# Performance work log

Measured on AMD Instinct MI355X. Metric: run time of the kernel, lower is better.

The kernel has to match this reference:

```python
import jax, jax.numpy as jnp
import numpy as np

B, U, N0, N1, E, H = 8, 8192, 64, 64, 128, 8
S = N0 * N1


def setup_inputs() -> dict:
    key = jax.random.key(0)
    ks = jax.random.split(key, 9)
    # regular grid over [-1, 1]^2 (meshgrid, 'ij' indexing)
    c0 = jnp.linspace(-1.0, 1.0, N0)
    c1 = jnp.linspace(-1.0, 1.0, N1)
    g0, g1 = jnp.meshgrid(c0, c1, indexing='ij')
    xc_on_grid = jnp.broadcast_to(jnp.stack([g0, g1], -1), (B, N0, N1, 2))
    xc_off_grid = jax.random.uniform(ks[0], (B, U, 2), minval=-1.0, maxval=1.0)
    zc_off_grid = jax.random.normal(ks[1], (B, U, E))
    zc_on_grid = jax.random.normal(ks[2], (B, N0, N1, E))
    latents = jax.random.normal(ks[3], (N0, N1, E))
    fake_embedding = jax.random.normal(ks[4], (E,))
    sc = 1.0 / np.sqrt(E).astype(np.float32)
    Wq = jax.random.normal(ks[5], (E, E)) * sc
    Wk = jax.random.normal(ks[6], (E, E)) * sc
    Wv = jax.random.normal(ks[7], (E, E)) * sc
    Wo = jax.random.normal(ks[8], (E, E)) * sc
    return dict(xc_off_grid=xc_off_grid, xc_on_grid=xc_on_grid,
                zc_off_grid=zc_off_grid, zc_on_grid=zc_on_grid,
                latents=latents, fake_embedding=fake_embedding,
                Wq=Wq, Wk=Wk, Wv=Wv, Wo=Wo, used_modality=0)


def _nearest_idx(x, x_grid):
    # nearest cell on a regular grid, flattened row-major (k=1 of nearest_gridded_neighbours)
    n0, n1 = x_grid.shape[1], x_grid.shape[2]
    c0 = x_grid[:, :, 0, 0]   # [B, n0]
    c1 = x_grid[:, 0, :, 1]   # [B, n1]
    sp0 = (c0[:, 1] - c0[:, 0])[:, None]
    sp1 = (c1[:, 1] - c1[:, 0])[:, None]
    i0 = jnp.clip(jnp.round((x[..., 0] - c0[:, :1]) / sp0), 0, n0 - 1)
    i1 = jnp.clip(jnp.round((x[..., 1] - c1[:, :1]) / sp1), 0, n1 - 1)
    return (i0 * n1 + i1).astype(jnp.int32)


def _cumcount(nearest):
    # duplicate-count within each grid cell via linear-recurrence associative scan
    # (same math as the torch complex-log scan: x_t = a_t*x_{t-1} + b_t, a=b=same-flag)
    sort_idx = jnp.argsort(nearest, axis=1, stable=True)
    ns = jnp.take_along_axis(nearest, sort_idx, axis=1)
    same = (ns == jnp.roll(ns, 1, axis=1)).astype(jnp.float32)
    same = same.at[:, 0].set(0.0)

    def combine(c1, c2):
        a1, b1 = c1
        a2, b2 = c2
        return a1 * a2, a2 * b1 + b2

    _, cc = jax.lax.associative_scan(combine, (same, same), axis=1)
    unsort = jnp.argsort(sort_idx, axis=1, stable=True)
    return jnp.take_along_axis(jnp.round(cc), unsort, axis=1).astype(jnp.int32)


def _mhca(q, kv, mask, Wq, Wk, Wv, Wo):
    # q: [N,1,E], kv: [N,P,E], mask: [N,1,P] (True = attend)
    N, P, Ed = kv.shape
    dh = Ed // H
    qh = (q @ Wq).reshape(N, 1, H, dh).transpose(0, 2, 1, 3)
    kh = (kv @ Wk).reshape(N, P, H, dh).transpose(0, 2, 1, 3)
    vh = (kv @ Wv).reshape(N, P, H, dh).transpose(0, 2, 1, 3)
    scores = jnp.einsum('nhqd,nhkd->nhqk', qh, kh) / jnp.sqrt(jnp.asarray(dh, qh.dtype))
    scores = jnp.where(mask[:, None, :, :], scores, -jnp.inf)
    attn = jax.nn.softmax(scores, axis=-1)
    out = jnp.einsum('nhqk,nhkd->nhqd', attn, vh)
    return out.transpose(0, 2, 1, 3).reshape(N, 1, Ed) @ Wo


def reference(xc_off_grid, xc_on_grid, zc_off_grid, zc_on_grid, latents,
              fake_embedding, Wq, Wk, Wv, Wo, used_modality):
    # PseudoTokenGridEncoder.forward, no-coarsening branch, used_modality=OFF_GRID
    Bb, Uu, Ee = zc_off_grid.shape
    n0, n1 = xc_on_grid.shape[1], xc_on_grid.shape[2]
    Ss = n0 * n1
    nearest = _nearest_idx(xc_off_grid, xc_on_grid)         # [B, U]
    cumcount = _cumcount(nearest)                           # [B, U]
    max_patch = int(jnp.max(cumcount)) + 2                  # data-dependent (eager)
    rows = nearest.reshape(-1) + jnp.repeat(jnp.arange(Bb) * Ss, Uu)
    cols = cumcount.reshape(-1)
    grid_stacked = jnp.zeros((Bb * Ss, max_patch, Ee), zc_off_grid.dtype)
    grid_stacked = grid_stacked.at[rows, cols].set(zc_off_grid.reshape(Bb * Uu, Ee))
    grid_stacked = grid_stacked.at[:, -1].set(fake_embedding)  # OFF_GRID -> fake token
    valid = jnp.zeros((Bb * Ss, max_patch), bool)
    valid = valid.at[rows, cols].set(True).at[:, -1].set(True)
    latent_flat = jnp.broadcast_to(latents.reshape(1, Ss, Ee), (Bb, Ss, Ee)).reshape(Bb * Ss, 1, Ee)
    out = _mhca(latent_flat, grid_stacked, valid[:, None, :], Wq, Wk, Wv, Wo)
    z_grid = out.reshape(Bb, n0, n1, Ee)
    return xc_on_grid, z_grid
```

## Files before the change

### kernel.cpp

```cpp
#include <hip/hip_runtime.h>
#include <hip/hip_bf16.h>

#define NB 8
#define NU 8192
#define GN0 64
#define GN1 64
#define NS 4096
#define NE 128
#define NH 8
#define CAP 20
#define NPTS (NB * NU)
#define NCELL (NB * NS)
#define OUT0 (NB * GN0 * GN1 * 2)


typedef __attribute__((ext_vector_type(8))) short short8v;
typedef __attribute__((ext_vector_type(4))) float float4v;

static __device__ inline unsigned pk2(float a, float b) {
  __hip_bfloat16 x = __float2bfloat16(a), y = __float2bfloat16(b);
  return ((unsigned)*(unsigned short*)&y << 16) | *(unsigned short*)&x;
}
static __device__ inline float bfs(short v) {
  unsigned u = (unsigned)(unsigned short)v << 16;
  return __builtin_bit_cast(float, u);
}

__global__ __launch_bounds__(256) void setup_kernel(
    const float* __restrict__ xc_on, const float* __restrict__ fake,
    const float* __restrict__ Wk, const float* __restrict__ Wv,
    const float* __restrict__ Wo,
    float* __restrict__ out, int* __restrict__ counts,
    float* __restrict__ fakeKV, __hip_bfloat16* __restrict__ Wt,
    __hip_bfloat16* __restrict__ Wot) {
  int t = threadIdx.x;
  int blk = blockIdx.x;
  if (blk < 64) {
    int idx = blk * 256 + t;
    ((float4*)out)[idx] = ((const float4*)xc_on)[idx];
    if (idx < NCELL / 4) ((int4*)counts)[idx] = int4{0, 0, 0, 0};
    return;
  }
  if (blk == 64) {
    __shared__ float frow[NE];
    if (t < NE) frow[t] = fake[t];
    __syncthreads();
    int e = t & 127, half = t >> 7;
    const float* W = half ? Wv : Wk;
    float acc = 0.f;
    for (int j = 0; j < NE; ++j) acc += frow[j] * W[j * NE + e];
    fakeKV[half * NE + e] = acc;
    return;
  }
  {
    int flat = (blk - 65) * 256 + t;
    int j = flat >> 7, e = flat & 127;
    Wt[e * NE + j] = __float2bfloat16(Wv[flat]);
    Wt[(128 + e) * NE + j] = __float2bfloat16(Wk[flat]);
    Wot[e * NE + j] = __float2bfloat16(Wo[flat]);
  }
}

__global__ __launch_bounds__(256) void vgemm_qf_kernel(
    const float* __restrict__ z, const float* __restrict__ xc_off,
    const float* __restrict__ xc_on, const __hip_bfloat16* __restrict__ Wt,
    const float* __restrict__ latents, const float* __restrict__ Wq,
    int* __restrict__ counts, unsigned short* __restrict__ lists,
    __hip_bfloat16* __restrict__ Vb, __hip_bfloat16* __restrict__ Kb,
    float* __restrict__ qf) {
  __shared__ __hip_bfloat16 zb[64 * 136];
  int tid = threadIdx.x;
  if ((int)blockIdx.x >= 1024) {
    float* lrow = (float*)zb;
    int s0 = ((int)blockIdx.x - 1024) * 8;
    for (int i = tid; i < 8 * NE; i += 256)
      lrow[i] = latents[(size_t)s0 * NE + i];
    __syncthreads();
    for (int i = tid; i < 8 * NE; i += 256) {
      int sl = i >> 7, e = i & 127;
      float acc = 0.f;
      for (int j = 0; j < NE; ++j) acc += lrow[sl * NE + j] * Wq[j * NE + e];
      qf[(size_t)(s0 + sl) * NE + e] = acc;
    }
    return;
  }
  int blk = ((int)blockIdx.x & 7) * 128 + ((int)blockIdx.x >> 3);
  size_t row0 = (size_t)blk * 64;
  for (int n = 0; n < 8; ++n) {
    int flat = n * 1024 + tid * 4;
    int r = flat >> 7, c = flat & 127;
    float4 v = *(const float4*)&z[(row0 + r) * NE + c];
    uint2 u = {pk2(v.x, v.y), pk2(v.z, v.w)};
    *(uint2*)&zb[r * 136 + c] = u;
  }
  if (tid < 64) {
    int p = (int)row0 + tid;
    int b = p >> 13;
    const float* g = xc_on + (size_t)b * (GN0 * GN1 * 2);
    float c00 = g[0], c01 = g[GN1 * 2], c10 = g[1], c11 = g[3];
    float x0 = xc_off[(size_t)p * 2 + 0];
    float x1 = xc_off[(size_t)p * 2 + 1];
    float f0 = rintf((x0 - c00) / (c01 - c00));
    float f1 = rintf((x1 - c10) / (c11 - c10));
    int i0 = (int)fminf(fmaxf(f0, 0.f), 63.f);
    int i1 = (int)fminf(fmaxf(f1, 0.f), 63.f);
    int cell = b * NS + i0 * GN1 + i1;
    int pos = atomicAdd(&counts[cell], 1);
    if (pos < CAP) lists[cell * CAP + pos] = (unsigned short)p;
  }
  __syncthreads();
  int wid = tid >> 6, l = tid & 63;
  int lr = l & 15, lk = l >> 4;
  const short* zl = (const short*)zb;
  const short* Wg = (const short*)Wt;
  float4v acc[4][4] = {};
  short8v bfrag[4][4];
#pragma unroll
  for (int ct = 0; ct < 4; ++ct) {
    int col = wid * 64 + ct * 16 + lr;
#pragma unroll
    for (int ks = 0; ks < 4; ++ks)
      bfrag[ct][ks] = *(const short8v*)&Wg[col * NE + ks * 32 + lk * 8];
  }
#pragma unroll
  for (int ks = 0; ks < 4; ++ks)
#pragma unroll
    for (int st = 0; st < 4; ++st) {
      short8v a = *(const short8v*)&zl[(st * 16 + lr) * 136 + ks * 32 + lk * 8];
#pragma unroll
      for (int ct = 0; ct < 4; ++ct)
        acc[st][ct] = __builtin_amdgcn_mfma_f32_16x16x32_bf16(a, bfrag[ct][ks], acc[st][ct], 0, 0, 0);
    }
  __hip_bfloat16* dst = (wid < 2) ? Vb : Kb;
  int cb = (wid & 1) * 64;
#pragma unroll
  for (int st = 0; st < 4; ++st)
#pragma unroll
    for (int ct = 0; ct < 4; ++ct)
#pragma unroll
      for (int r = 0; r < 4; ++r) {
        size_t row = row0 + st * 16 + lk * 4 + r;
        int col = cb + ct * 16 + lr;
        dst[row * NE + col] = __float2bfloat16(acc[st][ct][r]);
      }
}

__global__ __launch_bounds__(256) void attn_wo_kernel(
    const __hip_bfloat16* __restrict__ Vb, const __hip_bfloat16* __restrict__ Kb,
    const float* __restrict__ qf, const float* __restrict__ fakeKV,
    const int* __restrict__ counts, const unsigned short* __restrict__ lists,
    const __hip_bfloat16* __restrict__ Wot, float* __restrict__ out) {
  __shared__ __hip_bfloat16 ob[16 * 136];
  __shared__ float sc[4][4][24][8];
  __shared__ unsigned short pl[4][4][24];
  int tid = threadIdx.x, w = tid >> 6, l = tid & 63;
  int g = l >> 4, i = l & 15;
  int blk = ((int)blockIdx.x & 7) * 256 + ((int)blockIdx.x >> 3);
  int row = w * 4 + g;
  int cell = blk * 16 + row;
  int s = cell & (NS - 1);
  int cnt = min(counts[cell], CAP);
  for (int t = i; t < cnt; t += 16)
    pl[w][g][t] = lists[cell * CAP + t];
  int d0 = i * 8;
  float4 qa = *(const float4*)&qf[(size_t)s * NE + d0];
  float4 qb = *(const float4*)&qf[(size_t)s * NE + d0 + 4];
  __builtin_amdgcn_wave_barrier();
  for (int t = 0; t < cnt; ++t) {
    int pid = pl[w][g][t];
    short8v kv = *(const short8v*)(const short*)(Kb + (size_t)pid * NE + d0);
    float p = qa.x * bfs(kv[0]) + qa.y * bfs(kv[1]) + qa.z * bfs(kv[2]) + qa.w * bfs(kv[3])
            + qb.x * bfs(kv[4]) + qb.y * bfs(kv[5]) + qb.z * bfs(kv[6]) + qb.w * bfs(kv[7]);
    p += __shfl_xor(p, 1);
    if ((i & 1) == 0) sc[w][g][t][i >> 1] = p * 0.25f;
  }
  {
    float4 fa = *(const float4*)&fakeKV[d0];
    float4 fb = *(const float4*)&fakeKV[d0 + 4];
    float p = qa.x * fa.x + qa.y * fa.y + qa.z * fa.z + qa.w * fa.w
            + qb.x * fb.x + qb.y * fb.y + qb.z * fb.z + qb.w * fb.w;
    p += __shfl_xor(p, 1);
    if ((i & 1) == 0) sc[w][g][cnt][i >> 1] = p * 0.25f;
  }
  __builtin_amdgcn_wave_barrier();
  if (i < 8) {
    int T = cnt + 1;
    float m = -1e30f;
    for (int t = 0; t < T; ++t) m = fmaxf(m, sc[w][g][t][i]);
    float sum = 0.f;
    for (int t = 0; t < T; ++t) {
      float e = __expf(sc[w][g][t][i] - m);
      sum += e;
      sc[w][g][t][i] = e;
    }
    float inv = 1.f / sum;
    for (int t = 0; t < T; ++t) sc[w][g][t][i] *= inv;
  }
  __builtin_amdgcn_wave_barrier();
  int h = i >> 1;
  float va[8] = {0.f, 0.f, 0.f, 0.f, 0.f, 0.f, 0.f, 0.f};
  for (int t = 0; t < cnt; ++t) {
    int pid = pl[w][g][t];
    short8v vv = *(const short8v*)(const short*)(Vb + (size_t)pid * NE + d0);
    float wt = sc[w][g][t][h];
#pragma unroll
    for (int j = 0; j < 8; ++j) va[j] += wt * bfs(vv[j]);
  }
  {
    float4 fa = *(const float4*)&fakeKV[NE + d0];
    float4 fb = *(const float4*)&fakeKV[NE + d0 + 4];
    float wt = sc[w][g][cnt][h];
    va[0] += wt * fa.x; va[1] += wt * fa.y; va[2] += wt * fa.z; va[3] += wt * fa.w;
    va[4] += wt * fb.x; va[5] += wt * fb.y; va[6] += wt * fb.z; va[7] += wt * fb.w;
  }
  {
    uint4 u = {pk2(va[0], va[1]), pk2(va[2], va[3]),
               pk2(va[4], va[5]), pk2(va[6], va[7])};
    *(uint4*)&ob[row * 136 + d0] = u;
  }
  __syncthreads();
  int lr = l & 15, lk = l >> 4;
  const short* ol = (const short*)ob;
  const short* Wg = (const short*)Wot;
  short8v afr[4];
#pragma unroll
  for (int ks = 0; ks < 4; ++ks)
    afr[ks] = *(const short8v*)&ol[lr * 136 + ks * 32 + lk * 8];
  float4v acc[2] = {};
#pragma unroll
  for (int ct = 0; ct < 2; ++ct) {
    int col = (w * 2 + ct) * 16 + lr;
#pragma unroll
    for (int ks = 0; ks < 4; ++ks) {
      short8v bfr = *(const short8v*)&Wg[col * NE + ks * 32 + lk * 8];
      acc[ct] = __builtin_amdgcn_mfma_f32_16x16x32_bf16(afr[ks], bfr, acc[ct], 0, 0, 0);
    }
  }
  float* base = out + (size_t)OUT0 + (size_t)blk * 16 * NE;
#pragma unroll
  for (int ct = 0; ct < 2; ++ct)
#pragma unroll
    for (int r = 0; r < 4; ++r) {
      int orow = lk * 4 + r;
      int col = (w * 2 + ct) * 16 + lr;
      base[(size_t)orow * NE + col] = acc[ct][r];
    }
}

extern "C" void kernel_launch(void* const* d_in, const int* in_sizes, int n_in,
                              void* d_out, int out_size, void* d_ws, size_t ws_size,
                              hipStream_t stream) {
  const float* xc_off  = (const float*)d_in[0];
  const float* xc_on   = (const float*)d_in[1];
  const float* zc_off  = (const float*)d_in[2];
  const float* latents = (const float*)d_in[4];
  const float* fake    = (const float*)d_in[5];
  const float* Wq      = (const float*)d_in[6];
  const float* Wk      = (const float*)d_in[7];
  const float* Wv      = (const float*)d_in[8];
  const float* Wo      = (const float*)d_in[9];
  float* out = (float*)d_out;

  char* ws = (char*)d_ws;
  int*            counts = (int*)(ws);
  unsigned short* lists  = (unsigned short*)(ws + 131072);
  float*          qf     = (float*)(ws + 1441792);
  float*          fakeKV = (float*)(ws + 3538944);
  __hip_bfloat16* Wt     = (__hip_bfloat16*)(ws + 3539968);
  __hip_bfloat16* Wot    = (__hip_bfloat16*)(ws + 3605504);
  __hip_bfloat16* Vb     = (__hip_bfloat16*)(ws + 3638272);
  __hip_bfloat16* Kb     = (__hip_bfloat16*)(ws + 20415488);

  hipLaunchKernelGGL(setup_kernel, dim3(129), dim3(256), 0, stream,
                     xc_on, fake, Wk, Wv, Wo, out, counts, fakeKV, Wt, Wot);
  hipLaunchKernelGGL(vgemm_qf_kernel, dim3(1536), dim3(256), 0, stream,
                     zc_off, xc_off, xc_on, Wt, latents, Wq,
                     counts, lists, Vb, Kb, qf);
  hipLaunchKernelGGL(attn_wo_kernel, dim3(NCELL / 16), dim3(256), 0, stream,
                     Vb, Kb, qf, fakeKV, counts, lists, Wot, out);
}
```

Baseline: 59.50 us.

## Halve GEMM tile rows and prefetch first four K/V rows in attention

The V/K projection kernel now handles 32 rows per block instead of 64, doubling the grid size to give more blocks and better occupancy. The attention kernel drops the shared-memory staging of point lists and instead issues the first four K and V row gathers up front, so their latency overlaps. The remaining points still go through the original loop. This costs more registers per thread, and in the GEMM each block reloads its weight fragments for only half the work.

```diff
diff --git a/kernel.cpp b/kernel.cpp
--- a/kernel.cpp
+++ b/kernel.cpp
@@ -24,6 +24,10 @@
 static __device__ inline float bfs(short v) {
   unsigned u = (unsigned)(unsigned short)v << 16;
   return __builtin_bit_cast(float, u);
+}
+static __device__ inline float dot8(float4 qa, float4 qb, short8v kv) {
+  return qa.x * bfs(kv[0]) + qa.y * bfs(kv[1]) + qa.z * bfs(kv[2]) + qa.w * bfs(kv[3])
+       + qb.x * bfs(kv[4]) + qb.y * bfs(kv[5]) + qb.z * bfs(kv[6]) + qb.w * bfs(kv[7]);
 }
 
 __global__ __launch_bounds__(256) void setup_kernel(
@@ -68,11 +72,11 @@
     int* __restrict__ counts, unsigned short* __restrict__ lists,
     __hip_bfloat16* __restrict__ Vb, __hip_bfloat16* __restrict__ Kb,
     float* __restrict__ qf) {
-  __shared__ __hip_bfloat16 zb[64 * 136];
+  __shared__ __hip_bfloat16 zb[32 * 136];
   int tid = threadIdx.x;
-  if ((int)blockIdx.x >= 1024) {
+  if ((int)blockIdx.x >= 2048) {
     float* lrow = (float*)zb;
-    int s0 = ((int)blockIdx.x - 1024) * 8;
+    int s0 = ((int)blockIdx.x - 2048) * 8;
     for (int i = tid; i < 8 * NE; i += 256)
       lrow[i] = latents[(size_t)s0 * NE + i];
     __syncthreads();
@@ -84,16 +88,16 @@
     }
     return;
   }
-  int blk = ((int)blockIdx.x & 7) * 128 + ((int)blockIdx.x >> 3);
-  size_t row0 = (size_t)blk * 64;
-  for (int n = 0; n < 8; ++n) {
+  int blk = ((int)blockIdx.x & 7) * 256 + ((int)blockIdx.x >> 3);
+  size_t row0 = (size_t)blk * 32;
+  for (int n = 0; n < 4; ++n) {
     int flat = n * 1024 + tid * 4;
     int r = flat >> 7, c = flat & 127;
     float4 v = *(const float4*)&z[(row0 + r) * NE + c];
     uint2 u = {pk2(v.x, v.y), pk2(v.z, v.w)};
     *(uint2*)&zb[r * 136 + c] = u;
   }
-  if (tid < 64) {
+  if (tid < 32) {
     int p = (int)row0 + tid;
     int b = p >> 13;
     const float* g = xc_on + (size_t)b * (GN0 * GN1 * 2);
@@ -113,7 +117,7 @@
   int lr = l & 15, lk = l >> 4;
   const short* zl = (const short*)zb;
   const short* Wg = (const short*)Wt;
-  float4v acc[4][4] = {};
+  float4v acc[2][4] = {};
   short8v bfrag[4][4];
 #pragma unroll
   for (int ct = 0; ct < 4; ++ct) {
@@ -125,7 +129,7 @@
 #pragma unroll
   for (int ks = 0; ks < 4; ++ks)
 #pragma unroll
-    for (int st = 0; st < 4; ++st) {
+    for (int st = 0; st < 2; ++st) {
       short8v a = *(const short8v*)&zl[(st * 16 + lr) * 136 + ks * 32 + lk * 8];
 #pragma unroll
       for (int ct = 0; ct < 4; ++ct)
@@ -134,7 +138,7 @@
   __hip_bfloat16* dst = (wid < 2) ? Vb : Kb;
   int cb = (wid & 1) * 64;
 #pragma unroll
-  for (int st = 0; st < 4; ++st)
+  for (int st = 0; st < 2; ++st)
 #pragma unroll
     for (int ct = 0; ct < 4; ++ct)
 #pragma unroll
@@ -152,7 +156,6 @@
     const __hip_bfloat16* __restrict__ Wot, float* __restrict__ out) {
   __shared__ __hip_bfloat16 ob[16 * 136];
   __shared__ float sc[4][4][24][8];
-  __shared__ unsigned short pl[4][4][24];
   int tid = threadIdx.x, w = tid >> 6, l = tid & 63;
   int g = l >> 4, i = l & 15;
   int blk = ((int)blockIdx.x & 7) * 256 + ((int)blockIdx.x >> 3);
@@ -160,17 +163,40 @@
   int cell = blk * 16 + row;
   int s = cell & (NS - 1);
   int cnt = min(counts[cell], CAP);
-  for (int t = i; t < cnt; t += 16)
-    pl[w][g][t] = lists[cell * CAP + t];
   int d0 = i * 8;
   float4 qa = *(const float4*)&qf[(size_t)s * NE + d0];
   float4 qb = *(const float4*)&qf[(size_t)s * NE + d0 + 4];
-  __builtin_amdgcn_wave_barrier();
-  for (int t = 0; t < cnt; ++t) {
-    int pid = pl[w][g][t];
-    short8v kv = *(const short8v*)(const short*)(Kb + (size_t)pid * NE + d0);
-    float p = qa.x * bfs(kv[0]) + qa.y * bfs(kv[1]) + qa.z * bfs(kv[2]) + qa.w * bfs(kv[3])
-            + qb.x * bfs(kv[4]) + qb.y * bfs(kv[5]) + qb.z * bfs(kv[6]) + qb.w * bfs(kv[7]);
+  int pid0 = cnt > 0 ? (int)lists[cell * CAP + 0] : 0;
+  int pid1 = cnt > 1 ? (int)lists[cell * CAP + 1] : 0;
+  int pid2 = cnt > 2 ? (int)lists[cell * CAP + 2] : 0;
+  int pid3 = cnt > 3 ? (int)lists[cell * CAP + 3] : 0;
+  const short* Kbs = (const short*)Kb;
+  const short* Vbs = (const short*)Vb;
+  short8v k0 = *(const short8v*)&Kbs[(size_t)pid0 * NE + d0];
+  short8v k1 = *(const short8v*)&Kbs[(size_t)pid1 * NE + d0];
+  short8v k2 = *(const short8v*)&Kbs[(size_t)pid2 * NE + d0];
+  short8v k3 = *(const short8v*)&Kbs[(size_t)pid3 * NE + d0];
+  short8v v0 = *(const short8v*)&Vbs[(size_t)pid0 * NE + d0];
+  short8v v1 = *(const short8v*)&Vbs[(size_t)pid1 * NE + d0];
+  short8v v2 = *(const short8v*)&Vbs[(size_t)pid2 * NE + d0];
+  short8v v3 = *(const short8v*)&Vbs[(size_t)pid3 * NE + d0];
+  {
+    float p0 = dot8(qa, qb, k0), p1 = dot8(qa, qb, k1);
+    float p2 = dot8(qa, qb, k2), p3 = dot8(qa, qb, k3);
+    p0 += __shfl_xor(p0, 1); p1 += __shfl_xor(p1, 1);
+    p2 += __shfl_xor(p2, 1); p3 += __shfl_xor(p3, 1);
+    if ((i & 1) == 0) {
+      int hh = i >> 1;
+      if (cnt > 0) sc[w][g][0][hh] = p0 * 0.25f;
+      if (cnt > 1) sc[w][g][1][hh] = p1 * 0.25f;
+      if (cnt > 2) sc[w][g][2][hh] = p2 * 0.25f;
+      if (cnt > 3) sc[w][g][3][hh] = p3 * 0.25f;
+    }
+  }
+  for (int t = 4; t < cnt; ++t) {
+    int pid = (int)lists[cell * CAP + t];
+    short8v kv = *(const short8v*)&Kbs[(size_t)pid * NE + d0];
+    float p = dot8(qa, qb, kv);
     p += __shfl_xor(p, 1);
     if ((i & 1) == 0) sc[w][g][t][i >> 1] = p * 0.25f;
   }
@@ -199,9 +225,18 @@
   __builtin_amdgcn_wave_barrier();
   int h = i >> 1;
   float va[8] = {0.f, 0.f, 0.f, 0.f, 0.f, 0.f, 0.f, 0.f};
-  for (int t = 0; t < cnt; ++t) {
-    int pid = pl[w][g][t];
-    short8v vv = *(const short8v*)(const short*)(Vb + (size_t)pid * NE + d0);
+  {
+    float w0 = cnt > 0 ? sc[w][g][0][h] : 0.f;
+    float w1 = cnt > 1 ? sc[w][g][1][h] : 0.f;
+    float w2 = cnt > 2 ? sc[w][g][2][h] : 0.f;
+    float w3 = cnt > 3 ? sc[w][g][3][h] : 0.f;
+#pragma unroll
+    for (int j = 0; j < 8; ++j)
+      va[j] = w0 * bfs(v0[j]) + w1 * bfs(v1[j]) + w2 * bfs(v2[j]) + w3 * bfs(v3[j]);
+  }
+  for (int t = 4; t < cnt; ++t) {
+    int pid = (int)lists[cell * CAP + t];
+    short8v vv = *(const short8v*)&Vbs[(size_t)pid * NE + d0];
     float wt = sc[w][g][t][h];
 #pragma unroll
     for (int j = 0; j < 8; ++j) va[j] += wt * bfs(vv[j]);
@@ -273,7 +308,7 @@
 
   hipLaunchKernelGGL(setup_kernel, dim3(129), dim3(256), 0, stream,
                      xc_on, fake, Wk, Wv, Wo, out, counts, fakeKV, Wt, Wot);
-  hipLaunchKernelGGL(vgemm_qf_kernel, dim3(1536), dim3(256), 0, stream,
+  hipLaunchKernelGGL(vgemm_qf_kernel, dim3(2560), dim3(256), 0, stream,
                      zc_off, xc_off, xc_on, Wt, latents, Wq,
                      counts, lists, Vb, Kb, qf);
   hipLaunchKernelGGL(attn_wo_kernel, dim3(NCELL / 16), dim3(256), 0, stream,
```

Result: slower. 68.40 us (+14.9%).
